# Performance work log

Hardware: AMD Instinct MI355X
Metric: run time of the kernel (lower is better)

Reference implementation:

```python
import jax, jax.numpy as jnp
import numpy as np

VOCAB = 30001  # vocab_size + 1
EMB = 64
CHAR = 50
RNN = 128
TAGS = 9
B, T = 256, 512
D_IN = EMB + CHAR  # 114


def lstm_scan(x, Wx, Wh, b):
    # x: [T, B, D]; Keras LSTM gate order i, f, g(c), o; sigmoid/tanh activations.
    Bsz = x.shape[1]
    H = Wh.shape[0]
    def step(carry, xt):
        h, c = carry
        z = xt @ Wx + h @ Wh + b  # [B, 4H]
        i, f, g, o = jnp.split(z, 4, axis=-1)
        c = jax.nn.sigmoid(f) * c + jax.nn.sigmoid(i) * jnp.tanh(g)
        h = jax.nn.sigmoid(o) * jnp.tanh(c)
        return (h, c), h
    init = (jnp.zeros((Bsz, H), x.dtype), jnp.zeros((Bsz, H), x.dtype))
    _, hs = jax.lax.scan(step, init, x)
    return hs  # [T, B, H]


def crf_log_likelihood(logits, labels, lengths, trans):
    # logits: [B,T,K]; labels: [B,T] int; lengths: [B] int; trans: [K,K]
    Bsz, Tlen, K = logits.shape
    mask = (jnp.arange(Tlen)[None, :] < lengths[:, None]).astype(logits.dtype)  # [B,T]
    # gold path score: unary + pairwise transition terms
    unary = jnp.take_along_axis(logits, labels[..., None], axis=-1)[..., 0]  # [B,T]
    unary_score = jnp.sum(unary * mask, axis=1)
    binary = trans[labels[:, :-1], labels[:, 1:]]  # [B,T-1]
    binary_score = jnp.sum(binary * mask[:, 1:], axis=1)
    seq_score = unary_score + binary_score
    # forward algorithm (log-domain scan over time)
    logits_t = jnp.transpose(logits, (1, 0, 2))  # [T,B,K]
    mask_t = jnp.transpose(mask[:, 1:])          # [T-1,B]
    def step(alpha, inp):
        logit_t, m = inp
        new = jax.nn.logsumexp(alpha[:, :, None] + trans[None], axis=1) + logit_t
        alpha = jnp.where(m[:, None] > 0, new, alpha)
        return alpha, None
    alpha, _ = jax.lax.scan(step, logits_t[0], (logits_t[1:], mask_t))
    log_norm = jax.nn.logsumexp(alpha, axis=1)
    log_norm = jnp.where(lengths > 0, log_norm, jnp.zeros_like(log_norm))
    return seq_score - log_norm


def setup_inputs() -> dict:
    key = jax.random.key(0)
    ks = jax.random.split(key, 12)
    inputs = jax.random.randint(ks[0], (B, T), 0, 30000, dtype=jnp.int32)
    char_embeddings = jax.random.normal(ks[1], (B, T, CHAR), dtype=jnp.float32)
    labels = jax.random.randint(ks[2], (B, T), 0, TAGS, dtype=jnp.int32)
    E = 0.1 * jax.random.normal(ks[3], (VOCAB, EMB), dtype=jnp.float32)
    s_in = 1.0 / np.sqrt(D_IN)
    s_h = 1.0 / np.sqrt(RNN)
    Wx_f = s_in * jax.random.normal(ks[4], (D_IN, 4 * RNN), dtype=jnp.float32)
    Wh_f = s_h * jax.random.normal(ks[5], (RNN, 4 * RNN), dtype=jnp.float32)
    b_f = jnp.zeros((4 * RNN,), jnp.float32)
    Wx_b = s_in * jax.random.normal(ks[6], (D_IN, 4 * RNN), dtype=jnp.float32)
    Wh_b = s_h * jax.random.normal(ks[7], (RNN, 4 * RNN), dtype=jnp.float32)
    b_b = jnp.zeros((4 * RNN,), jnp.float32)
    Wd = (1.0 / np.sqrt(2 * RNN)) * jax.random.normal(ks[8], (2 * RNN, TAGS), dtype=jnp.float32)
    bd = jnp.zeros((TAGS,), jnp.float32)
    transition = jax.random.uniform(ks[9], (TAGS, TAGS), dtype=jnp.float32)
    return {"inputs": inputs, "char_embeddings": char_embeddings, "labels": labels,
            "E": E, "Wx_f": Wx_f, "Wh_f": Wh_f, "b_f": b_f,
            "Wx_b": Wx_b, "Wh_b": Wh_b, "b_b": b_b,
            "Wd": Wd, "bd": bd, "transition": transition}


def reference(inputs, char_embeddings, labels, E, Wx_f, Wh_f, b_f, Wx_b, Wh_b, b_b, Wd, bd, transition):
    emb = E[inputs]                                      # [B,T,64]
    x = jnp.concatenate([emb, char_embeddings], axis=2)  # [B,T,114]
    xt = jnp.transpose(x, (1, 0, 2))                     # [T,B,114]
    h_f = lstm_scan(xt, Wx_f, Wh_f, b_f)                 # [T,B,128]
    h_b = lstm_scan(xt[::-1], Wx_b, Wh_b, b_b)[::-1]     # [T,B,128]
    out = jnp.concatenate([h_f, h_b], axis=-1)           # [T,B,256]
    logits = jnp.transpose(out, (1, 0, 2)) @ Wd + bd     # [B,T,9]
    lengths = jnp.sum((labels != 0).astype(jnp.int32), axis=1)
    log_likelihood = crf_log_likelihood(logits, labels, lengths, transition)
    return log_likelihood, transition
```

## Files before the change

### kernel.cpp

```cpp
#include <hip/hip_runtime.h>

#define BB   256
#define TT   512
#define EMBD 64
#define CHARD 50
#define DIN  114
#define RNN  128
#define NG   512
#define TAGS 9

typedef __bf16 bf16x8 __attribute__((ext_vector_type(8)));
typedef float  f32x4  __attribute__((ext_vector_type(4)));

static __device__ __forceinline__ unsigned short f2bf(float f) {
  unsigned int u = __float_as_uint(f);
  unsigned int r = (u + 0x7FFFu + ((u >> 16) & 1u)) >> 16;
  return (unsigned short)r;
}
static __device__ __forceinline__ void gl_lds16(const void* g, void* l) {
  __builtin_amdgcn_global_load_lds(
      (const __attribute__((address_space(1))) unsigned int*)g,
      (__attribute__((address_space(3))) unsigned int*)l, 16, 0, 0);
}

__global__ void k_build_x(const int* __restrict__ inp, const float* __restrict__ ch,
                          const float* __restrict__ E, unsigned short* __restrict__ x) {
  int idx = blockIdx.x * 256 + threadIdx.x;
  int k   = idx & 127;
  int row = idx >> 7;
  float v;
  if (k < EMBD)      v = E[inp[row] * EMBD + k];
  else if (k < DIN)  v = ch[row * CHARD + (k - EMBD)];
  else               v = 0.f;
  x[idx] = f2bf(v);
}

__global__ void k_prep_w(const float* __restrict__ Wx_f, const float* __restrict__ Wh_f,
                         const float* __restrict__ Wx_b, const float* __restrict__ Wh_b,
                         const float* __restrict__ Wd,
                         unsigned short* __restrict__ WxT, unsigned short* __restrict__ WhT,
                         unsigned short* __restrict__ WdT) {
  if (blockIdx.x == 512) {
    for (int i = threadIdx.x; i < 16 * 256; i += 256) {
      int n = i >> 8, k = i & 255;
      WdT[i] = (n < TAGS) ? f2bf(Wd[k * TAGS + n]) : (unsigned short)0;
    }
    return;
  }
  int idx = blockIdx.x * 256 + threadIdx.x;
  int dir = idx >> 16;
  int rem = idx & 65535;
  int n   = rem >> 7;
  int kk  = rem & 127;
  const float* Wx = dir ? Wx_b : Wx_f;
  const float* Wh = dir ? Wh_b : Wh_f;
  WxT[idx] = (kk < DIN) ? f2bf(Wx[kk * NG + n]) : (unsigned short)0;
  WhT[idx] = f2bf(Wh[kk * NG + n]);
}

__global__ void k_lengths(const int* __restrict__ labels, int* __restrict__ lengths) {
  int b = blockIdx.x, lane = threadIdx.x;
  int cnt = 0;
  for (int t = lane; t < TT; t += 64) cnt += (labels[b * TT + t] != 0);
  for (int o = 32; o > 0; o >>= 1) cnt += __shfl_down(cnt, o);
  if (lane == 0) lengths[b] = cnt;
}

__global__ __launch_bounds__(512, 2) void k_fused(
    const unsigned short* __restrict__ x,
    const unsigned short* __restrict__ WxT,
    const unsigned short* __restrict__ WhT,
    const float* __restrict__ b_f, const float* __restrict__ b_b,
    const float* __restrict__ zcons, float* __restrict__ zprod,
    unsigned short* __restrict__ hseq, float* __restrict__ cbuf,
    int lstm_n, int s0, int s1, int first, int zs0, int znsteps)
{
  __shared__ __align__(16) char LDS[32768];
  const int tid = threadIdx.x, w = tid >> 6, l = tid & 63;
  const int lq = l & 15, lg = l >> 4;

  if ((int)blockIdx.x < lstm_n) {
    const int wg = blockIdx.x, dir = wg >> 5, rg = wg & 31, b0 = rg * 8;
    const unsigned short* WhD = WhT + dir * (NG * 128);
    unsigned short* hout = hseq + (size_t)dir * ((size_t)BB * TT * 128);
    char* ring = LDS;

    bf16x8 wh[4][4];
    #pragma unroll
    for (int g = 0; g < 4; ++g)
      #pragma unroll
      for (int kt = 0; kt < 4; ++kt)
        wh[g][kt] = *reinterpret_cast<const bf16x8*>(
            WhD + (g * RNN + w * 16 + lq) * 128 + kt * 32 + lg * 8);

    const int row7 = l & 7;
    int ro[4];
    #pragma unroll
    for (int kt = 0; kt < 4; ++kt)
      ro[kt] = (row7 * 16 + (((kt * 4) + lg) ^ row7)) * 16;

    int wo[2], rowr[2];
    #pragma unroll
    for (int rr = 0; rr < 2; ++rr) {
      rowr[rr] = (lg & 1) * 4 + (lg >> 1) * 2 + rr;
      int unit = rowr[rr] * 16 + ((w * 2 + (lq >> 3)) ^ rowr[rr]);
      wo[rr] = unit * 16 + (lq & 7) * 2;
    }
    const int hidden = w * 16 + lq;

    if (tid < 128) {
      int row = tid >> 4, h16 = tid & 15;
      int unit = row * 16 + (h16 ^ row);
      if (first) {
        *reinterpret_cast<f32x4*>(ring + 7 * 2048 + unit * 16) = f32x4{0.f, 0.f, 0.f, 0.f};
      } else {
        int tprev = dir ? (TT - s0) : (s0 - 1);
        bf16x8 v = *reinterpret_cast<const bf16x8*>(
            hout + ((size_t)(b0 + row) * TT + tprev) * 128 + h16 * 8);
        *reinterpret_cast<bf16x8*>(ring + 7 * 2048 + unit * 16) = v;
      }
    }
    float c[2];
    #pragma unroll
    for (int rr = 0; rr < 2; ++rr)
      c[rr] = first ? 0.f : cbuf[(size_t)(dir * BB + b0 + rowr[rr]) * RNN + hidden];
    __syncthreads();

    const float* zQ = zcons + (size_t)(((dir * 32 + rg) * 8 + w) * 2 + (lg & 1)) * 256;
    f32x4 zc[4];
    if (lg < 2) {
      #pragma unroll
      for (int g = 0; g < 4; ++g)
        zc[g] = *reinterpret_cast<const f32x4*>(zQ + g * 64 + lq * 4);
    }

    auto gather = [&](int sp) {
      int h16 = tid & 15, tc = (tid >> 4) & 3, row = tid >> 6;
      int ss = sp + tc, t = dir ? (TT - 1 - ss) : ss;
      bf16x8 v = *reinterpret_cast<const bf16x8*>(
          ring + (ss & 7) * 2048 + (row * 16 + (h16 ^ row)) * 16);
      *reinterpret_cast<bf16x8*>(hout + ((size_t)(b0 + row) * TT + t) * 128 + h16 * 8) = v;
    };

    for (int s = s0; s < s1; ++s) {
      f32x4 acc[4];
      #pragma unroll
      for (int g = 0; g < 4; ++g)
        acc[g] = (lg < 2) ? zc[g] : f32x4{0.f, 0.f, 0.f, 0.f};
      {
        int sn = (s + 1 < s1) ? (s + 1) : (s1 - 1);
        if (lg < 2) {
          const float* zp = zQ + (size_t)(sn - s0) * 262144;
          #pragma unroll
          for (int g = 0; g < 4; ++g)
            zc[g] = *reinterpret_cast<const f32x4*>(zp + g * 64 + lq * 4);
        }
      }

      const char* rb = ring + ((s - 1) & 7) * 2048;
      bf16x8 hf[4];
      #pragma unroll
      for (int kt = 0; kt < 4; ++kt)
        hf[kt] = *reinterpret_cast<const bf16x8*>(rb + ro[kt]);
      #pragma unroll
      for (int kt = 0; kt < 4; ++kt)
        #pragma unroll
        for (int g = 0; g < 4; ++g)
          acc[g] = __builtin_amdgcn_mfma_f32_16x16x32_bf16(hf[kt], wh[g][kt], acc[g], 0, 0, 0);

      if ((s & 3) == 0 && s > s0) gather(s - 4);

      float sw_[4][2];
      #pragma unroll
      for (int g = 0; g < 4; ++g)
        #pragma unroll
        for (int rr = 0; rr < 2; ++rr) {
          float d = acc[g][2 + rr], sv = acc[g][2 + rr];
          asm volatile("v_permlane32_swap_b32 %0, %1" : "+v"(d), "+v"(sv));
          sw_[g][rr] = d;
        }

      char* wslot = ring + (s & 7) * 2048;
      #pragma unroll
      for (int rr = 0; rr < 2; ++rr) {
        float zi = (lg < 2) ? acc[0][rr] : sw_[0][rr];
        float zf = (lg < 2) ? acc[1][rr] : sw_[1][rr];
        float zg = (lg < 2) ? acc[2][rr] : sw_[2][rr];
        float zo = (lg < 2) ? acc[3][rr] : sw_[3][rr];
        zi = fminf(20.f, fmaxf(-20.f, zi));
        zf = fminf(20.f, fmaxf(-20.f, zf));
        zg = fminf(20.f, fmaxf(-20.f, zg));
        zo = fminf(20.f, fmaxf(-20.f, zo));
        float ei = __expf(-zi), ef = __expf(-zf), eo = __expf(-zo);
        float g2 = __expf(2.f * zg);
        float P   = (1.f + ei) * (g2 + 1.f);
        float efp = 1.f + ef;
        float cn  = (c[rr] * P + efp * (g2 - 1.f)) * __builtin_amdgcn_rcpf(efp * P);
        c[rr] = cn;
        float cc = fminf(20.f, fmaxf(-20.f, cn));
        float ec = __expf(2.f * cc);
        float hn = (ec - 1.f) * __builtin_amdgcn_rcpf((1.f + eo) * (ec + 1.f));
        *reinterpret_cast<unsigned short*>(wslot + wo[rr]) = f2bf(hn);
      }
      __builtin_amdgcn_sched_barrier(0);
      asm volatile("s_waitcnt lgkmcnt(0)" ::: "memory");
      __builtin_amdgcn_s_barrier();
      __builtin_amdgcn_sched_barrier(0);
    }

    gather(s1 - 4);
    #pragma unroll
    for (int rr = 0; rr < 2; ++rr)
      cbuf[(size_t)(dir * BB + b0 + rowr[rr]) * RNN + hidden] = c[rr];
  } else {
    if (znsteps <= 0) return;
    const int TCHN = znsteps >> 4;
    const int zb = blockIdx.x - lstm_n;
    const int per = 16 * TCHN;
    const int dir = zb / per;
    const int rem = zb % per;
    const int rg2 = rem / TCHN, tch = rem % TCHN;
    const int b0p = rg2 * 16;
    const int sb  = zs0 + tch * 16;

    const unsigned short* WxD = WxT + dir * (NG * 128);
    const float* bias = dir ? b_b : b_f;
    unsigned short* xr = (unsigned short*)LDS;

    bf16x8 wx[4][4];
    float  bs[4];
    #pragma unroll
    for (int g = 0; g < 4; ++g) {
      int n = g * RNN + w * 16 + lq;
      bs[g] = bias[n];
      #pragma unroll
      for (int kt = 0; kt < 4; ++kt)
        wx[g][kt] = *reinterpret_cast<const bf16x8*>(WxD + n * 128 + kt * 32 + lg * 8);
    }

    auto stage = [&](int ci) {
      int buf = ci & 1;
      #pragma unroll
      for (int jj = 0; jj < 2; ++jj) {
        int idx = w * 2 + jj, sc = idx >> 2, kt = idx & 3;
        int s = sb + ci * 4 + sc;
        int t = dir ? (TT - 1 - s) : s;
        gl_lds16(x + ((size_t)(b0p + lq) * TT + t) * 128 + kt * 32 + lg * 8,
                 xr + buf * 8192 + sc * 2048 + kt * 512);
      }
    };

    stage(0);
    for (int ci = 0; ci < 4; ++ci) {
      __syncthreads();
      if (ci < 3) stage(ci + 1);
      int buf = ci & 1;
      #pragma unroll
      for (int sc = 0; sc < 4; ++sc) {
        int s = sb + ci * 4 + sc;
        bf16x8 xf[4];
        #pragma unroll
        for (int kt = 0; kt < 4; ++kt)
          xf[kt] = *reinterpret_cast<const bf16x8*>(xr + buf * 8192 + sc * 2048 + kt * 512 + l * 8);
        f32x4 acc[4];
        #pragma unroll
        for (int g = 0; g < 4; ++g) acc[g] = f32x4{bs[g], bs[g], bs[g], bs[g]};
        #pragma unroll
        for (int kt = 0; kt < 4; ++kt)
          #pragma unroll
          for (int g = 0; g < 4; ++g)
            acc[g] = __builtin_amdgcn_mfma_f32_16x16x32_bf16(xf[kt], wx[g][kt], acc[g], 0, 0, 0);
        float* zp = zprod + (size_t)(s - zs0) * 262144 +
                    (size_t)(((dir * 32 + rg2 * 2 + (lg >> 1)) * 8 + w) * 2 + (lg & 1)) * 256 +
                    lq * 4;
        #pragma unroll
        for (int g = 0; g < 4; ++g)
          *reinterpret_cast<f32x4*>(zp + g * 64) = acc[g];
      }
    }
  }
}

__global__ __launch_bounds__(256) void k_logits(const unsigned short* __restrict__ hseq,
                                                const unsigned short* __restrict__ WdT,
                                                const float* __restrict__ bd,
                                                float* __restrict__ logits,
                                                float* __restrict__ euk) {
  __shared__ __align__(16) unsigned short xt[2][16384];
  const int tid = threadIdx.x, wv = tid >> 6, l = tid & 63;
  const int lq = l & 15, lg = l >> 4;
  const size_t HS = (size_t)BB * TT * 128;

  bf16x8 wb[8];
  #pragma unroll
  for (int kt = 0; kt < 8; ++kt)
    wb[kt] = *reinterpret_cast<const bf16x8*>(WdT + lq * 256 + kt * 32 + lg * 8);
  float bdv = (lq < TAGS) ? bd[lq] : 0.f;

  auto stage = [&](int it, int buf) {
    int bt0 = blockIdx.x * 256 + it * 64;
    #pragma unroll
    for (int i = 0; i < 8; ++i) {
      int v = tid + i * 256;
      int g = v ^ ((v >> 5) & 7);
      int row = g >> 5, cu = g & 31;
      const unsigned short* src = (cu < 16)
          ? hseq + (size_t)(bt0 + row) * 128 + cu * 8
          : hseq + HS + (size_t)(bt0 + row) * 128 + (cu - 16) * 8;
      gl_lds16(src, &xt[buf][(i * 256 + wv * 64) * 8]);
    }
  };

  stage(0, 0);
  for (int it = 0; it < 4; ++it) {
    __syncthreads();
    if (it < 3) stage(it + 1, (it + 1) & 1);
    int buf = it & 1;
    int bt0 = blockIdx.x * 256 + it * 64;
    int r0 = wv * 16;
    bf16x8 af[8];
    #pragma unroll
    for (int kt = 0; kt < 8; ++kt) {
      int u = (r0 + lq) * 32 + kt * 4 + lg;
      af[kt] = *reinterpret_cast<const bf16x8*>(&xt[buf][(u ^ ((u >> 5) & 7)) * 8]);
    }
    f32x4 acc = f32x4{bdv, bdv, bdv, bdv};
    #pragma unroll
    for (int kt = 0; kt < 8; ++kt)
      acc = __builtin_amdgcn_mfma_f32_16x16x32_bf16(af[kt], wb[kt], acc, 0, 0, 0);
    float mr[4];
    #pragma unroll
    for (int r = 0; r < 4; ++r) {
      float v = (lq < TAGS) ? acc[r] : -1e30f;
      #pragma unroll
      for (int o = 1; o < 16; o <<= 1) v = fmaxf(v, __shfl_xor(v, o, 16));
      mr[r] = v;
    }
    #pragma unroll
    for (int r = 0; r < 4; ++r) {
      int rowi = bt0 + r0 + lg * 4 + r;
      if (lq < TAGS) logits[(size_t)rowi * TAGS + lq] = acc[r];
      if (lq < 12) {
        float val = (lq < TAGS) ? __expf(acc[r] - mr[r]) : ((lq == TAGS) ? mr[r] : 0.f);
        euk[(size_t)rowi * 12 + lq] = val;
      }
    }
  }
}

__global__ void k_score(const float* __restrict__ logits, const int* __restrict__ labels,
                        const int* __restrict__ lengths, const float* __restrict__ trans,
                        float* __restrict__ scbuf) {
  int b = blockIdx.x, lane = threadIdx.x;
  int len = lengths[b];
  const float* lg = logits + (size_t)b * TT * TAGS;
  const int*   lab = labels + b * TT;
  float sc = 0.f;
  for (int t = lane; t < TT; t += 64) {
    if (t < len) {
      sc += lg[t * TAGS + lab[t]];
      if (t >= 1) sc += trans[lab[t - 1] * TAGS + lab[t]];
    }
  }
  for (int o = 32; o > 0; o >>= 1) sc += __shfl_down(sc, o);
  if (lane == 0) scbuf[b] = sc;
}

__global__ __launch_bounds__(64) void k_crf2(const float* __restrict__ euk,
                                             const float* __restrict__ scbuf,
                                             const int* __restrict__ lengths,
                                             const float* __restrict__ trans,
                                             float* __restrict__ out) {
  int b = blockIdx.x * 64 + threadIdx.x;
  float Et[81];
  #pragma unroll
  for (int i = 0; i < 81; ++i) Et[i] = __expf(trans[i]);
  const float* ep = euk + (size_t)b * TT * 12;
  int len = lengths[b];

  float4 e0 = *reinterpret_cast<const float4*>(ep);
  float4 e1 = *reinterpret_cast<const float4*>(ep + 4);
  float4 e2 = *reinterpret_cast<const float4*>(ep + 8);
  float a[9] = {e0.x, e0.y, e0.z, e0.w, e1.x, e1.y, e1.z, e1.w, e2.x};
  float Ks = e2.y;
  int E2 = 0;
  float4 f0 = *reinterpret_cast<const float4*>(ep + 12);
  float4 f1 = *reinterpret_cast<const float4*>(ep + 16);
  float4 f2 = *reinterpret_cast<const float4*>(ep + 20);

  for (int t = 1; t < TT; ++t) {
    float eu[9] = {f0.x, f0.y, f0.z, f0.w, f1.x, f1.y, f1.z, f1.w, f2.x};
    float mt = f2.y;
    if (t + 1 < TT) {
      const float* np = ep + (size_t)(t + 1) * 12;
      f0 = *reinterpret_cast<const float4*>(np);
      f1 = *reinterpret_cast<const float4*>(np + 4);
      f2 = *reinterpret_cast<const float4*>(np + 8);
    }
    bool upd = (t < len);
    float an[9];
    #pragma unroll
    for (int j = 0; j < 9; ++j) {
      float s = a[0] * Et[j];
      #pragma unroll
      for (int i = 1; i < 9; ++i) s = fmaf(a[i], Et[i * 9 + j], s);
      an[j] = s * eu[j];
    }
    #pragma unroll
    for (int j = 0; j < 9; ++j) a[j] = upd ? an[j] : a[j];
    Ks += upd ? mt : 0.f;
    float s = fmaxf(fmaxf(fmaxf(a[0], a[1]), fmaxf(a[2], a[3])),
                    fmaxf(fmaxf(a[4], a[5]), fmaxf(a[6], a[7])));
    s = fmaxf(s, a[8]);
    int e;
    frexpf(s, &e);
    E2 += e;
    #pragma unroll
    for (int j = 0; j < 9; ++j) a[j] = ldexpf(a[j], -e);
  }
  float S = ((a[0] + a[1]) + (a[2] + a[3])) + ((a[4] + a[5]) + (a[6] + a[7])) + a[8];
  float ln = logf(S) + (float)E2 * 0.69314718056f + Ks;
  out[b] = (len > 0) ? (scbuf[b] - ln) : 0.f;
}

__global__ void k_copy_trans(const float* __restrict__ trans, float* __restrict__ out) {
  int i = threadIdx.x;
  if (i < TAGS * TAGS) out[BB + i] = trans[i];
}

extern "C" void kernel_launch(void* const* d_in, const int* in_sizes, int n_in,
                              void* d_out, int out_size, void* d_ws, size_t ws_size,
                              hipStream_t stream) {
  const int*   inp    = (const int*)d_in[0];
  const float* ch     = (const float*)d_in[1];
  const int*   labels = (const int*)d_in[2];
  const float* E      = (const float*)d_in[3];
  const float* Wx_f   = (const float*)d_in[4];
  const float* Wh_f   = (const float*)d_in[5];
  const float* b_f    = (const float*)d_in[6];
  const float* Wx_b   = (const float*)d_in[7];
  const float* Wh_b   = (const float*)d_in[8];
  const float* b_b    = (const float*)d_in[9];
  const float* Wd     = (const float*)d_in[10];
  const float* bd     = (const float*)d_in[11];
  const float* trans  = (const float*)d_in[12];
  float* out = (float*)d_out;

  unsigned short* x    = (unsigned short*)d_ws;
  unsigned short* hseq = x + (size_t)BB * TT * 128;
  unsigned short* WxT  = hseq + (size_t)2 * BB * TT * 128;
  unsigned short* WhT  = WxT + 2 * NG * 128;
  unsigned short* WdT  = WhT + 2 * NG * 128;
  float* logits        = (float*)(WdT + 16 * 256);
  float* euk           = logits + (size_t)BB * TT * TAGS;
  float* cbuf          = euk + (size_t)BB * TT * 12;
  float* scbuf         = cbuf + (size_t)2 * BB * RNN;
  int*   lengths       = (int*)(scbuf + BB);
  float* zbuf          = (float*)(lengths + 256);

  const size_t zoff = (size_t)((char*)zbuf - (char*)d_ws);
  int NP = 8;
  if (zoff + 2ull * (TT / 8)  * 1048576ull > ws_size) NP = 16;
  if (zoff + 2ull * (TT / 16) * 1048576ull > ws_size) NP = 32;
  const int L = TT / NP;
  const size_t zsl = (size_t)L * 262144;

  k_build_x<<<(BB * TT * 128) / 256, 256, 0, stream>>>(inp, ch, E, x);
  k_prep_w<<<513, 256, 0, stream>>>(Wx_f, Wh_f, Wx_b, Wh_b, Wd, WxT, WhT, WdT);
  k_lengths<<<BB, 64, 0, stream>>>(labels, lengths);

  k_fused<<<2 * 16 * (L / 16), 512, 0, stream>>>(x, WxT, WhT, b_f, b_b,
                                                 zbuf, zbuf, hseq, cbuf,
                                                 0, 0, 0, 1, 0, L);
  for (int p = 0; p < NP; ++p) {
    int nz = (p + 1 < NP) ? 2 * 16 * (L / 16) : 0;
    k_fused<<<64 + nz, 512, 0, stream>>>(
        x, WxT, WhT, b_f, b_b,
        zbuf + (size_t)(p & 1) * zsl,
        zbuf + (size_t)((p + 1) & 1) * zsl,
        hseq, cbuf,
        64, p * L, (p + 1) * L, (p == 0) ? 1 : 0, (p + 1) * L, nz ? L : 0);
  }

  k_logits<<<(BB * TT) / 256, 256, 0, stream>>>(hseq, WdT, bd, logits, euk);
  k_score<<<BB, 64, 0, stream>>>(logits, labels, lengths, trans, scbuf);
  k_crf2<<<BB / 64, 64, 0, stream>>>(euk, scbuf, lengths, trans, out);
  k_copy_trans<<<1, 128, 0, stream>>>(trans, out);
}
```

Before: 736.8 us.

## Store LSTM input projections in bf16 and parallelize CRF forward across time

The precomputed input-gate projections (z buffer) are now stored as bf16 instead of fp32, and prefetched two steps ahead. This halves the z buffer's traffic and footprint, which lets the launcher pick fewer, longer LSTM phases (fewer launches). The CRF forward algorithm is rewritten from one sequential 511-step scan per batch row into a per-wave parallel scan. Each lane multiplies 8 scaled transition matrices, and the lanes then combine their products by 9x9 matrix multiplication over butterfly shuffles, shortening the serial dependency chain. The trade-offs are reduced precision in the gate pre-activations and many more FLOPs and registers (81-float matrices) in the CRF kernel.

```diff
diff --git a/kernel.cpp b/kernel.cpp
--- a/kernel.cpp
+++ b/kernel.cpp
@@ -11,6 +11,7 @@
 
 typedef __bf16 bf16x8 __attribute__((ext_vector_type(8)));
 typedef float  f32x4  __attribute__((ext_vector_type(4)));
+typedef unsigned int u32x2 __attribute__((ext_vector_type(2)));
 
 static __device__ __forceinline__ unsigned short f2bf(float f) {
   unsigned int u = __float_as_uint(f);
@@ -71,7 +72,7 @@
     const unsigned short* __restrict__ WxT,
     const unsigned short* __restrict__ WhT,
     const float* __restrict__ b_f, const float* __restrict__ b_b,
-    const float* __restrict__ zcons, float* __restrict__ zprod,
+    const unsigned short* __restrict__ zcons, unsigned short* __restrict__ zprod,
     unsigned short* __restrict__ hseq, float* __restrict__ cbuf,
     int lstm_n, int s0, int s1, int first, int zs0, int znsteps)
 {
@@ -126,12 +127,15 @@
       c[rr] = first ? 0.f : cbuf[(size_t)(dir * BB + b0 + rowr[rr]) * RNN + hidden];
     __syncthreads();
 
-    const float* zQ = zcons + (size_t)(((dir * 32 + rg) * 8 + w) * 2 + (lg & 1)) * 256;
-    f32x4 zc[4];
+    const unsigned short* zQ = zcons +
+        (size_t)(((dir * 32 + rg) * 8 + w) * 2 + (lg & 1)) * 256 + lq * 4;
+    u32x2 zA[4], zB[4];
     if (lg < 2) {
       #pragma unroll
-      for (int g = 0; g < 4; ++g)
-        zc[g] = *reinterpret_cast<const f32x4*>(zQ + g * 64 + lq * 4);
+      for (int g = 0; g < 4; ++g) zA[g] = *reinterpret_cast<const u32x2*>(zQ + g * 64);
+      const unsigned short* zp1 = zQ + (size_t)((s0 + 1 < s1) ? 1 : 0) * 262144;
+      #pragma unroll
+      for (int g = 0; g < 4; ++g) zB[g] = *reinterpret_cast<const u32x2*>(zp1 + g * 64);
     }
 
     auto gather = [&](int sp) {
@@ -145,15 +149,20 @@
     for (int s = s0; s < s1; ++s) {
       f32x4 acc[4];
       #pragma unroll
-      for (int g = 0; g < 4; ++g)
-        acc[g] = (lg < 2) ? zc[g] : f32x4{0.f, 0.f, 0.f, 0.f};
+      for (int g = 0; g < 4; ++g) {
+        unsigned int lo = zA[g][0], hi = zA[g][1];
+        f32x4 zv = f32x4{__uint_as_float(lo << 16), __uint_as_float(lo & 0xffff0000u),
+                         __uint_as_float(hi << 16), __uint_as_float(hi & 0xffff0000u)};
+        acc[g] = (lg < 2) ? zv : f32x4{0.f, 0.f, 0.f, 0.f};
+      }
       {
-        int sn = (s + 1 < s1) ? (s + 1) : (s1 - 1);
+        #pragma unroll
+        for (int g = 0; g < 4; ++g) zA[g] = zB[g];
+        int sn = (s + 2 < s1) ? (s + 2) : (s1 - 1);
         if (lg < 2) {
-          const float* zp = zQ + (size_t)(sn - s0) * 262144;
+          const unsigned short* zp = zQ + (size_t)(sn - s0) * 262144;
           #pragma unroll
-          for (int g = 0; g < 4; ++g)
-            zc[g] = *reinterpret_cast<const f32x4*>(zp + g * 64 + lq * 4);
+          for (int g = 0; g < 4; ++g) zB[g] = *reinterpret_cast<const u32x2*>(zp + g * 64);
         }
       }
 
@@ -270,12 +279,15 @@
           #pragma unroll
           for (int g = 0; g < 4; ++g)
             acc[g] = __builtin_amdgcn_mfma_f32_16x16x32_bf16(xf[kt], wx[g][kt], acc[g], 0, 0, 0);
-        float* zp = zprod + (size_t)(s - zs0) * 262144 +
-                    (size_t)(((dir * 32 + rg2 * 2 + (lg >> 1)) * 8 + w) * 2 + (lg & 1)) * 256 +
-                    lq * 4;
-        #pragma unroll
-        for (int g = 0; g < 4; ++g)
-          *reinterpret_cast<f32x4*>(zp + g * 64) = acc[g];
+        unsigned short* zp = zprod + (size_t)(s - zs0) * 262144 +
+            (size_t)(((dir * 32 + rg2 * 2 + (lg >> 1)) * 8 + w) * 2 + (lg & 1)) * 256 + lq * 4;
+        #pragma unroll
+        for (int g = 0; g < 4; ++g) {
+          ushort4 v;
+          v.x = f2bf(acc[g][0]); v.y = f2bf(acc[g][1]);
+          v.z = f2bf(acc[g][2]); v.w = f2bf(acc[g][3]);
+          *reinterpret_cast<ushort4*>(zp + g * 64) = v;
+        }
       }
     }
   }
@@ -366,61 +378,131 @@
   if (lane == 0) scbuf[b] = sc;
 }
 
-__global__ __launch_bounds__(64) void k_crf2(const float* __restrict__ euk,
-                                             const float* __restrict__ scbuf,
-                                             const int* __restrict__ lengths,
-                                             const float* __restrict__ trans,
-                                             float* __restrict__ out) {
-  int b = blockIdx.x * 64 + threadIdx.x;
+__global__ __launch_bounds__(256, 1) void k_crf2(const float* __restrict__ euk,
+                                                 const float* __restrict__ scbuf,
+                                                 const int* __restrict__ lengths,
+                                                 const float* __restrict__ trans,
+                                                 float* __restrict__ out) {
+  const int wv = threadIdx.x >> 6, lane = threadIdx.x & 63;
+  const int b = blockIdx.x * 4 + wv;
+  const float* ep = euk + (size_t)b * TT * 12;
+  const int len = lengths[b];
+  const int lim = (len < TT) ? len : TT;
+
   float Et[81];
   #pragma unroll
   for (int i = 0; i < 81; ++i) Et[i] = __expf(trans[i]);
-  const float* ep = euk + (size_t)b * TT * 12;
-  int len = lengths[b];
-
-  float4 e0 = *reinterpret_cast<const float4*>(ep);
-  float4 e1 = *reinterpret_cast<const float4*>(ep + 4);
-  float4 e2 = *reinterpret_cast<const float4*>(ep + 8);
-  float a[9] = {e0.x, e0.y, e0.z, e0.w, e1.x, e1.y, e1.z, e1.w, e2.x};
-  float Ks = e2.y;
-  int E2 = 0;
-  float4 f0 = *reinterpret_cast<const float4*>(ep + 12);
-  float4 f1 = *reinterpret_cast<const float4*>(ep + 16);
-  float4 f2 = *reinterpret_cast<const float4*>(ep + 20);
-
-  for (int t = 1; t < TT; ++t) {
-    float eu[9] = {f0.x, f0.y, f0.z, f0.w, f1.x, f1.y, f1.z, f1.w, f2.x};
-    float mt = f2.y;
-    if (t + 1 < TT) {
-      const float* np = ep + (size_t)(t + 1) * 12;
-      f0 = *reinterpret_cast<const float4*>(np);
-      f1 = *reinterpret_cast<const float4*>(np + 4);
-      f2 = *reinterpret_cast<const float4*>(np + 8);
-    }
-    bool upd = (t < len);
-    float an[9];
-    #pragma unroll
-    for (int j = 0; j < 9; ++j) {
-      float s = a[0] * Et[j];
-      #pragma unroll
-      for (int i = 1; i < 9; ++i) s = fmaf(a[i], Et[i * 9 + j], s);
-      an[j] = s * eu[j];
-    }
-    #pragma unroll
-    for (int j = 0; j < 9; ++j) a[j] = upd ? an[j] : a[j];
+
+  float P[81];
+  float Ks = 0.f;
+  int   E2 = 0;
+
+  const int t0 = 1 + lane * 8;
+  auto rec = [&](int t) { int tl = (t < TT) ? t : (TT - 1); return ep + (size_t)tl * 12; };
+
+  const float* p0 = rec(t0);
+  float4 A0 = *(const float4*)p0, A1 = *(const float4*)(p0 + 4), A2 = *(const float4*)(p0 + 8);
+  const float* p1 = rec(t0 + 1);
+  float4 B0 = *(const float4*)p1, B1 = *(const float4*)(p1 + 4), B2 = *(const float4*)(p1 + 8);
+
+  {
+    float eu[9] = {A0.x, A0.y, A0.z, A0.w, A1.x, A1.y, A1.z, A1.w, A2.x};
+    bool upd = t0 < lim;
+    #pragma unroll
+    for (int i = 0; i < 9; ++i)
+      #pragma unroll
+      for (int j = 0; j < 9; ++j)
+        P[i * 9 + j] = upd ? Et[i * 9 + j] * eu[j] : ((i == j) ? 1.f : 0.f);
+    Ks += upd ? A2.y : 0.f;
+    A0 = B0; A1 = B1; A2 = B2;
+    const float* pn = rec(t0 + 2);
+    B0 = *(const float4*)pn; B1 = *(const float4*)(pn + 4); B2 = *(const float4*)(pn + 8);
+  }
+
+  for (int s = 1; s < 8; ++s) {
+    float eu[9] = {A0.x, A0.y, A0.z, A0.w, A1.x, A1.y, A1.z, A1.w, A2.x};
+    float mt = A2.y;
+    bool upd = (t0 + s) < lim;
+    A0 = B0; A1 = B1; A2 = B2;
+    const float* pn = rec(t0 + s + 2);
+    B0 = *(const float4*)pn; B1 = *(const float4*)(pn + 4); B2 = *(const float4*)(pn + 8);
+    #pragma unroll
+    for (int i = 0; i < 9; ++i) {
+      float tmp[9];
+      #pragma unroll
+      for (int j = 0; j < 9; ++j) {
+        float a = P[i * 9 + 0] * Et[0 * 9 + j];
+        #pragma unroll
+        for (int k = 1; k < 9; ++k) a = fmaf(P[i * 9 + k], Et[k * 9 + j], a);
+        tmp[j] = a * eu[j];
+      }
+      #pragma unroll
+      for (int j = 0; j < 9; ++j) P[i * 9 + j] = upd ? tmp[j] : P[i * 9 + j];
+    }
     Ks += upd ? mt : 0.f;
-    float s = fmaxf(fmaxf(fmaxf(a[0], a[1]), fmaxf(a[2], a[3])),
-                    fmaxf(fmaxf(a[4], a[5]), fmaxf(a[6], a[7])));
-    s = fmaxf(s, a[8]);
-    int e;
-    frexpf(s, &e);
-    E2 += e;
-    #pragma unroll
-    for (int j = 0; j < 9; ++j) a[j] = ldexpf(a[j], -e);
-  }
-  float S = ((a[0] + a[1]) + (a[2] + a[3])) + ((a[4] + a[5]) + (a[6] + a[7])) + a[8];
-  float ln = logf(S) + (float)E2 * 0.69314718056f + Ks;
-  out[b] = (len > 0) ? (scbuf[b] - ln) : 0.f;
+  }
+
+  {
+    float m = P[0];
+    #pragma unroll
+    for (int e = 1; e < 81; ++e) m = fmaxf(m, P[e]);
+    int ex; frexpf(m, &ex);
+    #pragma unroll
+    for (int e = 0; e < 81; ++e) P[e] = ldexpf(P[e], -ex);
+    E2 += ex;
+  }
+
+  for (int d = 0; d < 6; ++d) {
+    int msk = 1 << d;
+    float Q[81];
+    #pragma unroll
+    for (int e = 0; e < 81; ++e) Q[e] = __shfl_xor(P[e], msk);
+    int   E2p = __shfl_xor(E2, msk);
+    float Ksp = __shfl_xor(Ks, msk);
+    bool late = (lane & msk) != 0;
+    #pragma unroll
+    for (int e = 0; e < 81; ++e) {
+      float a = P[e], q = Q[e];
+      P[e] = late ? q : a;
+      Q[e] = late ? a : q;
+    }
+    #pragma unroll
+    for (int i = 0; i < 9; ++i) {
+      float tmp[9];
+      #pragma unroll
+      for (int j = 0; j < 9; ++j) {
+        float a = P[i * 9 + 0] * Q[0 * 9 + j];
+        #pragma unroll
+        for (int k = 1; k < 9; ++k) a = fmaf(P[i * 9 + k], Q[k * 9 + j], a);
+        tmp[j] = a;
+      }
+      #pragma unroll
+      for (int j = 0; j < 9; ++j) P[i * 9 + j] = tmp[j];
+    }
+    E2 += E2p; Ks += Ksp;
+    float m = P[0];
+    #pragma unroll
+    for (int e = 1; e < 81; ++e) m = fmaxf(m, P[e]);
+    int ex; frexpf(m, &ex);
+    #pragma unroll
+    for (int e = 0; e < 81; ++e) P[e] = ldexpf(P[e], -ex);
+    E2 += ex;
+  }
+
+  float4 z0 = *(const float4*)ep, z1 = *(const float4*)(ep + 4), z2 = *(const float4*)(ep + 8);
+  float eu0[9] = {z0.x, z0.y, z0.z, z0.w, z1.x, z1.y, z1.z, z1.w, z2.x};
+  float alpha[9];
+  #pragma unroll
+  for (int j = 0; j < 9; ++j) {
+    float a = eu0[0] * P[0 * 9 + j];
+    #pragma unroll
+    for (int i = 1; i < 9; ++i) a = fmaf(eu0[i], P[i * 9 + j], a);
+    alpha[j] = a;
+  }
+  float S = ((alpha[0] + alpha[1]) + (alpha[2] + alpha[3])) +
+            ((alpha[4] + alpha[5]) + (alpha[6] + alpha[7])) + alpha[8];
+  float ln = logf(S) + (float)E2 * 0.69314718056f + Ks + z2.y;
+  if (lane == 0) out[b] = (len > 0) ? (scbuf[b] - ln) : 0.f;
 }
 
 __global__ void k_copy_trans(const float* __restrict__ trans, float* __restrict__ out) {
@@ -456,12 +538,15 @@
   float* cbuf          = euk + (size_t)BB * TT * 12;
   float* scbuf         = cbuf + (size_t)2 * BB * RNN;
   int*   lengths       = (int*)(scbuf + BB);
-  float* zbuf          = (float*)(lengths + 256);
+  unsigned short* zbuf = (unsigned short*)(lengths + 256);
 
   const size_t zoff = (size_t)((char*)zbuf - (char*)d_ws);
-  int NP = 8;
-  if (zoff + 2ull * (TT / 8)  * 1048576ull > ws_size) NP = 16;
-  if (zoff + 2ull * (TT / 16) * 1048576ull > ws_size) NP = 32;
+  int NP = 4;
+  const int cands[4] = {4, 8, 16, 32};
+  for (int i = 0; i < 4; ++i) {
+    NP = cands[i];
+    if (zoff + 2ull * (size_t)(TT / NP) * 524288ull <= ws_size) break;
+  }
   const int L = TT / NP;
   const size_t zsl = (size_t)L * 262144;
 
@@ -484,6 +569,6 @@
 
   k_logits<<<(BB * TT) / 256, 256, 0, stream>>>(hseq, WdT, bd, logits, euk);
   k_score<<<BB, 64, 0, stream>>>(logits, labels, lengths, trans, scbuf);
-  k_crf2<<<BB / 64, 64, 0, stream>>>(euk, scbuf, lengths, trans, out);
+  k_crf2<<<BB / 4, 256, 0, stream>>>(euk, scbuf, lengths, trans, out);
   k_copy_trans<<<1, 128, 0, stream>>>(trans, out);
 }
```

After: 605.6 us, median of 2. 17.8% less time.
